# Optimization experiments

Hardware: AMD Instinct MI355X
Metric: run time of the kernel (lower is better)

## Reference

```python
import jax, jax.numpy as jnp
import numpy as np

N, M = 2048, 2048
NODE_DIM = 64
HIDDEN_DIM = 64  # must equal NODE_DIM due to broadcast in msg = weights * h_r
LN_EPS = 1e-5


def setup_inputs() -> dict:
    key = jax.random.key(0)
    ks = jax.random.split(key, 14)
    s_edge1 = 1.0 / np.sqrt(4.0)
    s_edge2 = 1.0 / np.sqrt(HIDDEN_DIM)
    s_n1 = 1.0 / np.sqrt(NODE_DIM + HIDDEN_DIM)
    s_n2 = 1.0 / np.sqrt(NODE_DIM)
    return {
        "h_l": jax.random.normal(ks[0], (N, NODE_DIM), jnp.float32),
        "x_l": jax.random.normal(ks[1], (N, 3), jnp.float32),
        "h_r": jax.random.normal(ks[2], (M, NODE_DIM), jnp.float32),
        "x_r": jax.random.normal(ks[3], (M, 3), jnp.float32),
        # edge_mlp: Linear(4, hidden), SiLU, Linear(hidden, hidden)
        "W1": jax.random.uniform(ks[4], (4, HIDDEN_DIM), jnp.float32, -s_edge1, s_edge1),
        "b1": jax.random.uniform(ks[5], (HIDDEN_DIM,), jnp.float32, -s_edge1, s_edge1),
        "W2": jax.random.uniform(ks[6], (HIDDEN_DIM, HIDDEN_DIM), jnp.float32, -s_edge2, s_edge2),
        "b2": jax.random.uniform(ks[7], (HIDDEN_DIM,), jnp.float32, -s_edge2, s_edge2),
        # node_update: Linear(node+hidden, node), LayerNorm(node), SiLU, Linear(node, node)
        "Wn1": jax.random.uniform(ks[8], (NODE_DIM + HIDDEN_DIM, NODE_DIM), jnp.float32, -s_n1, s_n1),
        "bn1": jax.random.uniform(ks[9], (NODE_DIM,), jnp.float32, -s_n1, s_n1),
        "ln_g": jnp.ones((NODE_DIM,), jnp.float32),
        "ln_b": jnp.zeros((NODE_DIM,), jnp.float32),
        "Wn2": jax.random.uniform(ks[10], (NODE_DIM, NODE_DIM), jnp.float32, -s_n2, s_n2),
        "bn2": jax.random.uniform(ks[11], (NODE_DIM,), jnp.float32, -s_n2, s_n2),
    }


def _forward(h_l, x_l, h_r, x_r, W1, b1, W2, b2, Wn1, bn1, ln_g, ln_b, Wn2, bn2):
    # squared pairwise distances [N, M]
    d2 = jnp.sum((x_l[:, None, :] - x_r[None, :, :]) ** 2, axis=-1)
    dist_feat = jnp.exp(-d2 / 5.0)
    # chemical-property interaction matrices from last 3 node features
    l_p, r_p = h_l[:, -3:], h_r[:, -3:]
    hbond = l_p[:, 0:1] * r_p[:, 1:2].T + l_p[:, 1:2] * r_p[:, 0:1].T  # [N, M]
    hydro = l_p[:, 2:3] * r_p[:, 2:3].T                                # [N, M]
    edge_raw = jnp.stack([dist_feat, hbond, hydro, jnp.ones_like(d2)], axis=-1)  # [N, M, 4]
    # edge MLP -> sigmoid gating weights [N, M, H]
    e = jax.nn.silu(edge_raw @ W1 + b1) @ W2 + b2
    w = jax.nn.sigmoid(e)
    # weighted, normalized aggregation over M
    h_agg = jnp.einsum('nmh,mh->nh', w, h_r) / (jnp.sum(w, axis=1) + 1e-6)
    # node update MLP with LayerNorm
    z = jnp.concatenate([h_l, h_agg], axis=-1) @ Wn1 + bn1
    mu = jnp.mean(z, axis=-1, keepdims=True)
    var = jnp.var(z, axis=-1, keepdims=True)
    z = (z - mu) / jnp.sqrt(var + LN_EPS) * ln_g + ln_b
    z = jax.nn.silu(z) @ Wn2 + bn2
    return h_l + z


def reference(h_l, x_l, h_r, x_r, W1, b1, W2, b2, Wn1, bn1, ln_g, ln_b, Wn2, bn2):
    return _forward(h_l, x_l, h_r, x_r, W1, b1, W2, b2, Wn1, bn1, ln_g, ln_b, Wn2, bn2)
```

## Files before the change

kernel.cpp:

```cpp
#include <hip/hip_runtime.h>
#include <hip/hip_bf16.h>
#include <hip/hip_fp16.h>


#define NTOT 2048
#define MTOT 2048
#define MSPLIT 32
#define MCHUNK 64

typedef _Float16 f16x8 __attribute__((ext_vector_type(8)));
typedef float f32x4  __attribute__((ext_vector_type(4)));
typedef float f32x2  __attribute__((ext_vector_type(2)));
typedef int   i32x4  __attribute__((ext_vector_type(4)));

#define NL2E (-1.4426950408889634f)
#define C1E  (-0.2885390081777927f)

__device__ __forceinline__ float fast_exp2(float x) {
#if __has_builtin(__builtin_amdgcn_exp2f)
  return __builtin_amdgcn_exp2f(x);
#else
  return __exp2f(x);
#endif
}
__device__ __forceinline__ float fast_rcp(float x) {
#if __has_builtin(__builtin_amdgcn_rcpf)
  return __builtin_amdgcn_rcpf(x);
#else
  return 1.0f / x;
#endif
}
__device__ __forceinline__ float fast_rsq(float x) {
#if __has_builtin(__builtin_amdgcn_rsqf)
  return __builtin_amdgcn_rsqf(x);
#else
  return rsqrtf(x);
#endif
}
__device__ __forceinline__ f32x2 pk_fma(f32x2 a, f32x2 b, f32x2 c) {
  return __builtin_elementwise_fma(a, b, c);
}

__global__ __launch_bounds__(256, 2)
void edge_kernel(const float* __restrict__ h_l,
                 const float* __restrict__ x_l,
                 const float* __restrict__ h_r,
                 const float* __restrict__ x_r,
                 const float* __restrict__ W1,
                 const float* __restrict__ b1,
                 const float* __restrict__ W2,
                 const float* __restrict__ b2,
                 float* __restrict__ num_g,
                 float* __restrict__ den_g) {
  __shared__ float hrT[MCHUNK][64];
  __shared__ float xr_s[MCHUNK][8];

  const int tid  = threadIdx.x;
  const int wave = tid >> 6;
  const int lane = tid & 63;
  const int l15  = lane & 15;
  const int quad = lane >> 4;

  const int nblk   = blockIdx.x / MSPLIT;
  const int msplit = blockIdx.x % MSPLIT;
  const int n0     = nblk * 64 + wave * 16;
  const int mBase  = msplit * MCHUNK;

  const int nA = n0 + l15;
  const float xl0 = x_l[nA * 3 + 0];
  const float xl1 = x_l[nA * 3 + 1];
  const float xl2 = x_l[nA * 3 + 2];
  const float lp0 = h_l[nA * 64 + 61];
  const float lp1 = h_l[nA * 64 + 62];
  const float lp2 = h_l[nA * 64 + 63];

  __half2 w1d2[8], w1h2[8], w1y2[8], b1p2[8];
#pragma unroll
  for (int p = 0; p < 8; ++p) {
    const int j0 = 2 * p, j1 = 2 * p + 1;
    const int hA = (j0 < 8) ? (quad * 8 + j0) : (32 + quad * 8 + (j0 - 8));
    const int hB = (j1 < 8) ? (quad * 8 + j1) : (32 + quad * 8 + (j1 - 8));
    w1d2[p] = __floats2half2_rn(W1[0 * 64 + hA], W1[0 * 64 + hB]);
    w1h2[p] = __floats2half2_rn(W1[1 * 64 + hA], W1[1 * 64 + hB]);
    w1y2[p] = __floats2half2_rn(W1[2 * 64 + hA], W1[2 * 64 + hB]);
    b1p2[p] = __floats2half2_rn(b1[hA] + W1[3 * 64 + hA],
                                b1[hB] + W1[3 * 64 + hB]);
  }

  f16x8 Bfrag[4][2];
#pragma unroll
  for (int c = 0; c < 4; ++c) {
#pragma unroll
    for (int h = 0; h < 2; ++h) {
      f16x8 f;
#pragma unroll
      for (int j = 0; j < 8; ++j) {
        const int k = h * 32 + quad * 8 + j;
        f[j] = (_Float16)W2[k * 64 + c * 16 + l15];
      }
      Bfrag[c][h] = f;
    }
  }

  f32x2 b2c2[4];
#pragma unroll
  for (int c = 0; c < 4; ++c) {
    const float v = NL2E * b2[c * 16 + l15];
    b2c2[c] = f32x2{v, v};
  }

  for (int idx = tid; idx < MCHUNK * 64; idx += 256) {
    const int mm = idx >> 6, w = idx & 63;
    const int i = w >> 2, c = w & 3;
    hrT[mm][w] = h_r[(mBase + mm) * 64 + c * 16 + i];
  }
  for (int idx = tid; idx < MCHUNK * 8; idx += 256) {
    const int mm = idx >> 3, k = idx & 7;
    float v = 0.f;
    const int m = mBase + mm;
    if (k < 3)      v = x_r[m * 3 + k];
    else if (k < 6) v = h_r[m * 64 + 61 + (k - 3)];
    xr_s[mm][k] = v;
  }

  const f32x4 zero4 = {0.f, 0.f, 0.f, 0.f};
  const f32x2 one2 = {1.f, 1.f};
  const f32x2 nl2e2 = {NL2E, NL2E};
  const __half2 nl2eh = __float2half2_rn(NL2E);
  const __half2 oneh  = __float2half2_rn(1.0f);
  f32x2 numr2[4][2], denr2[4][2];
#pragma unroll
  for (int c = 0; c < 4; ++c)
#pragma unroll
    for (int h = 0; h < 2; ++h) {
      numr2[c][h] = f32x2{0.f, 0.f};
      denr2[c][h] = f32x2{0.f, 0.f};
    }

  __syncthreads();

#pragma unroll 2
  for (int ms = 0; ms < MCHUNK; ++ms) {
    const f32x4 xa = *(const f32x4*)&xr_s[ms][0];
    const f32x2 xb = *(const f32x2*)&xr_s[ms][4];
    const float dx = xl0 - xa[0], dy = xl1 - xa[1], dz = xl2 - xa[2];
    const float d2 = fmaf(dz, dz, fmaf(dy, dy, dx * dx));
    const float dist = fast_exp2(d2 * C1E);
    const float hb = fmaf(lp1, xa[3], lp0 * xb[0]);
    const float hy = lp2 * xb[1];
    const __half2 dist2 = __float2half2_rn(dist);
    const __half2 hb2 = __float2half2_rn(hb);
    const __half2 hy2 = __float2half2_rn(hy);

    __half2 s2[8];
#pragma unroll
    for (int p = 0; p < 8; ++p) {
      const __half2 t2 = __hfma2(dist2, w1d2[p],
                         __hfma2(hb2, w1h2[p],
                         __hfma2(hy2, w1y2[p], b1p2[p])));
      const __half2 a2 = __hmul2(t2, nl2eh);
      const __half2 e2 = h2exp2(a2);
      const __half2 dden = __hadd2(e2, oneh);
      const __half2 r2 = h2rcp(dden);
      s2[p] = __hmul2(t2, r2);
    }
    i32x4 p0, p1;
    p0.x = __builtin_bit_cast(int, s2[0]);  p0.y = __builtin_bit_cast(int, s2[1]);
    p0.z = __builtin_bit_cast(int, s2[2]);  p0.w = __builtin_bit_cast(int, s2[3]);
    p1.x = __builtin_bit_cast(int, s2[4]);  p1.y = __builtin_bit_cast(int, s2[5]);
    p1.z = __builtin_bit_cast(int, s2[6]);  p1.w = __builtin_bit_cast(int, s2[7]);
    const f16x8 A0 = __builtin_bit_cast(f16x8, p0);
    const f16x8 A1 = __builtin_bit_cast(f16x8, p1);

    f32x4 acc[4];
#pragma unroll
    for (int c = 0; c < 4; ++c) {
      acc[c] = __builtin_amdgcn_mfma_f32_16x16x32_f16(A0, Bfrag[c][0], zero4, 0, 0, 0);
      acc[c] = __builtin_amdgcn_mfma_f32_16x16x32_f16(A1, Bfrag[c][1], acc[c], 0, 0, 0);
    }

    const f32x4 hrv4 = *(const f32x4*)&hrT[ms][l15 * 4];
#pragma unroll
    for (int c = 0; c < 4; ++c) {
      const f32x2 hrv2 = {hrv4[c], hrv4[c]};
#pragma unroll
      for (int h = 0; h < 2; ++h) {
        const f32x2 a2 = {acc[c][2 * h], acc[c][2 * h + 1]};
        const f32x2 arg = pk_fma(a2, nl2e2, b2c2[c]);
        f32x2 e2;
        e2.x = fast_exp2(arg.x);
        e2.y = fast_exp2(arg.y);
        const f32x2 dden = e2 + one2;
        f32x2 w2;
        w2.x = fast_rcp(dden.x);
        w2.y = fast_rcp(dden.y);
        numr2[c][h] = pk_fma(w2, hrv2, numr2[c][h]);
        denr2[c][h] = denr2[c][h] + w2;
      }
    }
  }

#pragma unroll
  for (int c = 0; c < 4; ++c)
#pragma unroll
    for (int h = 0; h < 2; ++h)
#pragma unroll
      for (int k = 0; k < 2; ++k) {
        const int r = 2 * h + k;
        const int n = n0 + quad * 4 + r;
        const int h2 = c * 16 + l15;
        atomicAdd(&num_g[n * 64 + h2], k ? numr2[c][h].y : numr2[c][h].x);
        atomicAdd(&den_g[n * 64 + h2], k ? denr2[c][h].y : denr2[c][h].x);
      }
}

__global__ __launch_bounds__(256)
void node_kernel(const float* __restrict__ h_l,
                 const float* __restrict__ num_g,
                 const float* __restrict__ den_g,
                 const float* __restrict__ Wn1,
                 const float* __restrict__ bn1,
                 const float* __restrict__ ln_g,
                 const float* __restrict__ ln_b,
                 const float* __restrict__ Wn2,
                 const float* __restrict__ bn2,
                 float* __restrict__ out) {
  __shared__ float Wn1_s[128 * 64];
  __shared__ float Wn2_s[64 * 64];
  __shared__ float xbuf[4][128];
  __shared__ float zbuf[4][64];

  const int tid = threadIdx.x;
  for (int i = tid; i < 128 * 64; i += 256) Wn1_s[i] = Wn1[i];
  for (int i = tid; i < 64 * 64; i += 256) Wn2_s[i] = Wn2[i];

  const int wave = tid >> 6, lane = tid & 63;
  const int row = blockIdx.x * 4 + wave;

  const float hl = h_l[row * 64 + lane];
  const float dn = den_g[row * 64 + lane] + 1e-6f;
  const float hagg = num_g[row * 64 + lane] * fast_rcp(dn);
  xbuf[wave][lane] = hl;
  xbuf[wave][64 + lane] = hagg;
  __syncthreads();

  float t = bn1[lane];
#pragma unroll 8
  for (int k = 0; k < 128; ++k) t = fmaf(xbuf[wave][k], Wn1_s[k * 64 + lane], t);

  float s1 = t, s2 = t * t;
#pragma unroll
  for (int off = 32; off; off >>= 1) {
    s1 += __shfl_xor(s1, off);
    s2 += __shfl_xor(s2, off);
  }
  const float mu = s1 * 0.015625f;
  const float var = fmaf(s2, 0.015625f, -mu * mu);
  const float rs = fast_rsq(var + 1e-5f);
  const float zn = fmaf((t - mu) * rs, ln_g[lane], ln_b[lane]);
  const float sz = zn * fast_rcp(1.0f + fast_exp2(zn * NL2E));
  zbuf[wave][lane] = sz;
  __syncthreads();

  float o = bn2[lane];
#pragma unroll 8
  for (int k = 0; k < 64; ++k) o = fmaf(zbuf[wave][k], Wn2_s[k * 64 + lane], o);

  out[row * 64 + lane] = hl + o;
}

extern "C" void kernel_launch(void* const* d_in, const int* in_sizes, int n_in,
                              void* d_out, int out_size, void* d_ws, size_t ws_size,
                              hipStream_t stream) {
  const float* h_l = (const float*)d_in[0];
  const float* x_l = (const float*)d_in[1];
  const float* h_r = (const float*)d_in[2];
  const float* x_r = (const float*)d_in[3];
  const float* W1  = (const float*)d_in[4];
  const float* b1  = (const float*)d_in[5];
  const float* W2  = (const float*)d_in[6];
  const float* b2  = (const float*)d_in[7];
  const float* Wn1 = (const float*)d_in[8];
  const float* bn1 = (const float*)d_in[9];
  const float* lng = (const float*)d_in[10];
  const float* lnb = (const float*)d_in[11];
  const float* Wn2 = (const float*)d_in[12];
  const float* bn2 = (const float*)d_in[13];

  float* num_g = (float*)d_ws;
  float* den_g = num_g + (size_t)NTOT * 64;

  hipMemsetAsync(d_ws, 0, (size_t)NTOT * 64 * 2 * sizeof(float), stream);
  edge_kernel<<<dim3((NTOT / 64) * MSPLIT), dim3(256), 0, stream>>>(
      h_l, x_l, h_r, x_r, W1, b1, W2, b2, num_g, den_g);
  node_kernel<<<dim3(NTOT / 4), dim3(256), 0, stream>>>(
      h_l, num_g, den_g, Wn1, bn1, lng, lnb, Wn2, bn2, (float*)d_out);
}
```

Baseline: 217.4 us.

## Move W1/W2 fragments from registers to LDS and reload per iteration

Instead of holding the W2 MFMA B-fragments and the packed W1/b1 half2 weights in registers for the whole loop, the kernel stages them in shared memory in fragment-ready layout and reloads them every m-step. The layer-1 FMAs are expressed as 16-wide half vector FMAs, and the loop is kept from unrolling with a compiler memory barrier. The aim is to cut VGPR pressure so the kernel can sustain occupancy or avoid spills. The cost is extra LDS reads on every iteration and the loss of the 2x unroll, which could expose more latency.

```diff
diff --git a/kernel.cpp b/kernel.cpp
--- a/kernel.cpp
+++ b/kernel.cpp
@@ -8,10 +8,10 @@
 #define MSPLIT 32
 #define MCHUNK 64
 
-typedef _Float16 f16x8 __attribute__((ext_vector_type(8)));
+typedef _Float16 f16x8  __attribute__((ext_vector_type(8)));
+typedef _Float16 f16x16 __attribute__((ext_vector_type(16)));
 typedef float f32x4  __attribute__((ext_vector_type(4)));
 typedef float f32x2  __attribute__((ext_vector_type(2)));
-typedef int   i32x4  __attribute__((ext_vector_type(4)));
 
 #define NL2E (-1.4426950408889634f)
 #define C1E  (-0.2885390081777927f)
@@ -40,6 +40,11 @@
 __device__ __forceinline__ f32x2 pk_fma(f32x2 a, f32x2 b, f32x2 c) {
   return __builtin_elementwise_fma(a, b, c);
 }
+__device__ __forceinline__ f16x16 pk_fma16(f16x16 a, f16x16 b, f16x16 c) {
+  return __builtin_elementwise_fma(a, b, c);
+}
+
+union F16U { f16x16 v; __half2 h[8]; f16x8 a[2]; };
 
 __global__ __launch_bounds__(256, 2)
 void edge_kernel(const float* __restrict__ h_l,
@@ -54,6 +59,8 @@
                  float* __restrict__ den_g) {
   __shared__ float hrT[MCHUNK][64];
   __shared__ float xr_s[MCHUNK][8];
+  __shared__ __align__(16) _Float16 w2L[4096];
+  __shared__ __align__(16) _Float16 w1L[4 * 72];
 
   const int tid  = threadIdx.x;
   const int wave = tid >> 6;
@@ -74,41 +81,27 @@
   const float lp1 = h_l[nA * 64 + 62];
   const float lp2 = h_l[nA * 64 + 63];
 
-  __half2 w1d2[8], w1h2[8], w1y2[8], b1p2[8];
-#pragma unroll
-  for (int p = 0; p < 8; ++p) {
-    const int j0 = 2 * p, j1 = 2 * p + 1;
-    const int hA = (j0 < 8) ? (quad * 8 + j0) : (32 + quad * 8 + (j0 - 8));
-    const int hB = (j1 < 8) ? (quad * 8 + j1) : (32 + quad * 8 + (j1 - 8));
-    w1d2[p] = __floats2half2_rn(W1[0 * 64 + hA], W1[0 * 64 + hB]);
-    w1h2[p] = __floats2half2_rn(W1[1 * 64 + hA], W1[1 * 64 + hB]);
-    w1y2[p] = __floats2half2_rn(W1[2 * 64 + hA], W1[2 * 64 + hB]);
-    b1p2[p] = __floats2half2_rn(b1[hA] + W1[3 * 64 + hA],
-                                b1[hB] + W1[3 * 64 + hB]);
-  }
-
-  f16x8 Bfrag[4][2];
-#pragma unroll
-  for (int c = 0; c < 4; ++c) {
-#pragma unroll
-    for (int h = 0; h < 2; ++h) {
-      f16x8 f;
-#pragma unroll
-      for (int j = 0; j < 8; ++j) {
-        const int k = h * 32 + quad * 8 + j;
-        f[j] = (_Float16)W2[k * 64 + c * 16 + l15];
-      }
-      Bfrag[c][h] = f;
-    }
-  }
-
-  f32x2 b2c2[4];
-#pragma unroll
-  for (int c = 0; c < 4; ++c) {
-    const float v = NL2E * b2[c * 16 + l15];
-    b2c2[c] = f32x2{v, v};
-  }
-
+  for (int idx = tid; idx < 4096; idx += 256) {
+    const int j = idx & 7, i15 = (idx >> 3) & 15;
+    const int q = (idx >> 7) & 3, hh = (idx >> 9) & 1, c = (idx >> 10) & 3;
+    const int k = hh * 32 + q * 8 + j;
+    w2L[idx] = (_Float16)W2[k * 64 + c * 16 + i15];
+  }
+  {
+    const int idx = tid;
+    if (idx < 256) {
+      const int q = idx >> 6, r = idx & 63;
+      const int arr = r >> 4, pp = (r >> 1) & 7, hilo = r & 1;
+      const int j = 2 * pp + hilo;
+      const int hcol = (j < 8) ? (q * 8 + j) : (32 + q * 8 + (j - 8));
+      float v;
+      if (arr == 0)      v = W1[hcol];
+      else if (arr == 1) v = W1[64 + hcol];
+      else if (arr == 2) v = W1[128 + hcol];
+      else               v = b1[hcol] + W1[192 + hcol];
+      w1L[q * 72 + arr * 16 + pp * 2 + hilo] = (_Float16)v;
+    }
+  }
   for (int idx = tid; idx < MCHUNK * 64; idx += 256) {
     const int mm = idx >> 6, w = idx & 63;
     const int i = w >> 2, c = w & 3;
@@ -123,6 +116,13 @@
     xr_s[mm][k] = v;
   }
 
+  f32x2 b2c2[4];
+#pragma unroll
+  for (int c = 0; c < 4; ++c) {
+    const float v = NL2E * b2[c * 16 + l15];
+    b2c2[c] = f32x2{v, v};
+  }
+
   const f32x4 zero4 = {0.f, 0.f, 0.f, 0.f};
   const f32x2 one2 = {1.f, 1.f};
   const f32x2 nl2e2 = {NL2E, NL2E};
@@ -139,8 +139,13 @@
 
   __syncthreads();
 
-#pragma unroll 2
+  const f16x16* w1q = (const f16x16*)(w1L + quad * 72);
+  const f16x8*  w2p = (const f16x8*)w2L + (quad * 16 + l15);
+
+#pragma unroll 1
   for (int ms = 0; ms < MCHUNK; ++ms) {
+    asm volatile("" ::: "memory");
+
     const f32x4 xa = *(const f32x4*)&xr_s[ms][0];
     const f32x2 xb = *(const f32x2*)&xr_s[ms][4];
     const float dx = xl0 - xa[0], dy = xl1 - xa[1], dz = xl2 - xa[2];
@@ -151,32 +156,34 @@
     const __half2 dist2 = __float2half2_rn(dist);
     const __half2 hb2 = __float2half2_rn(hb);
     const __half2 hy2 = __float2half2_rn(hy);
-
-    __half2 s2[8];
+    F16U distv, hbv, hyv;
+#pragma unroll
+    for (int p = 0; p < 8; ++p) { distv.h[p] = dist2; hbv.h[p] = hb2; hyv.h[p] = hy2; }
+
+    const f16x16 wd = w1q[0];
+    const f16x16 wh = w1q[1];
+    const f16x16 wy = w1q[2];
+    const f16x16 wb = w1q[3];
+    F16U T;
+    T.v = pk_fma16(distv.v, wd, pk_fma16(hbv.v, wh, pk_fma16(hyv.v, wy, wb)));
+
+    F16U S;
 #pragma unroll
     for (int p = 0; p < 8; ++p) {
-      const __half2 t2 = __hfma2(dist2, w1d2[p],
-                         __hfma2(hb2, w1h2[p],
-                         __hfma2(hy2, w1y2[p], b1p2[p])));
-      const __half2 a2 = __hmul2(t2, nl2eh);
+      const __half2 a2 = __hmul2(T.h[p], nl2eh);
       const __half2 e2 = h2exp2(a2);
-      const __half2 dden = __hadd2(e2, oneh);
-      const __half2 r2 = h2rcp(dden);
-      s2[p] = __hmul2(t2, r2);
-    }
-    i32x4 p0, p1;
-    p0.x = __builtin_bit_cast(int, s2[0]);  p0.y = __builtin_bit_cast(int, s2[1]);
-    p0.z = __builtin_bit_cast(int, s2[2]);  p0.w = __builtin_bit_cast(int, s2[3]);
-    p1.x = __builtin_bit_cast(int, s2[4]);  p1.y = __builtin_bit_cast(int, s2[5]);
-    p1.z = __builtin_bit_cast(int, s2[6]);  p1.w = __builtin_bit_cast(int, s2[7]);
-    const f16x8 A0 = __builtin_bit_cast(f16x8, p0);
-    const f16x8 A1 = __builtin_bit_cast(f16x8, p1);
+      const __half2 dd = __hadd2(e2, oneh);
+      const __half2 r2 = h2rcp(dd);
+      S.h[p] = __hmul2(T.h[p], r2);
+    }
+    const f16x8 A0 = S.a[0];
+    const f16x8 A1 = S.a[1];
 
     f32x4 acc[4];
 #pragma unroll
     for (int c = 0; c < 4; ++c) {
-      acc[c] = __builtin_amdgcn_mfma_f32_16x16x32_f16(A0, Bfrag[c][0], zero4, 0, 0, 0);
-      acc[c] = __builtin_amdgcn_mfma_f32_16x16x32_f16(A1, Bfrag[c][1], acc[c], 0, 0, 0);
+      acc[c] = __builtin_amdgcn_mfma_f32_16x16x32_f16(A0, w2p[(c * 2 + 0) * 64], zero4, 0, 0, 0);
+      acc[c] = __builtin_amdgcn_mfma_f32_16x16x32_f16(A1, w2p[(c * 2 + 1) * 64], acc[c], 0, 0, 0);
     }
 
     const f32x4 hrv4 = *(const f32x4*)&hrT[ms][l15 * 4];
```

After: 227.3 us. 4.6% more time.
